# Optimization experiments

Measured on AMD Instinct MI355X. Metric: run time of the kernel, lower is better.

## Reference

```python
import jax, jax.numpy as jnp
import numpy as np


def _oct_table():
    # e_i * e_j = sgn[i,j] * e_{idx[i,j]}  (standard Fano-plane octonion table)
    idx = np.zeros((8, 8), dtype=np.int32)
    sgn = np.zeros((8, 8), dtype=np.float32)
    for j in range(8):
        idx[0, j] = j; sgn[0, j] = 1.0
    for i in range(1, 8):
        idx[i, 0] = i; sgn[i, 0] = 1.0
        idx[i, i] = 0; sgn[i, i] = -1.0
    for (a, b, c) in [(1, 2, 3), (1, 4, 5), (1, 7, 6), (2, 4, 6), (2, 5, 7), (3, 4, 7), (3, 6, 5)]:
        for (p, q, r) in ((a, b, c), (b, c, a), (c, a, b)):
            idx[p, q] = r; sgn[p, q] = 1.0
            idx[q, p] = r; sgn[q, p] = -1.0
    # For output part k and weight part i, J[k,i] is the unique input part j
    # with e_i*e_j = SG[k,i]*e_k.
    J = np.zeros((8, 8), dtype=np.int32)
    SG = np.zeros((8, 8), dtype=np.float32)
    for i in range(8):
        for j in range(8):
            k = idx[i, j]
            J[k, i] = j; SG[k, i] = sgn[i, j]
    return J, SG

_J, _SG = _oct_table()
_SGj = jnp.asarray(_SG)


def ternary_quant(W):
    # BitNet-style: per-matrix abs-mean scale, round+clip to {-1,0,1}, rescale.
    scale = jnp.mean(jnp.abs(W), axis=(1, 2), keepdims=True)
    return jnp.clip(jnp.round(W / (scale + 1e-8)), -1.0, 1.0) * scale


def oct_linear(x, W):
    # x: [B,T,Cin] (8 concatenated parts), W: [8, Pout, Pin]
    B, T, Cin = x.shape
    xp = x.reshape(B, T, 8, Cin // 8)
    Wq = ternary_quant(W)
    outs = []
    for k in range(8):  # fixed structural loop over octonion components
        xm = _SGj[k][None, None, :, None] * xp[:, :, _J[k], :]  # [B,T,8,Pin]
        outs.append(jnp.einsum('btip,iop->bto', xm, Wq))
    return jnp.concatenate(outs, axis=-1)  # [B,T,8*Pout]


def rmsnorm(x, w, eps=1e-6):
    return x * jax.lax.rsqrt(jnp.mean(x * x, axis=-1, keepdims=True) + eps) * w


def rope(x, cos, sin):
    # x: [B,T,H,D] with complex pairs (even, odd); cos/sin: [T,D/2]
    xr, xi = x[..., 0::2], x[..., 1::2]
    c = cos[None, :, None, :]
    s = sin[None, :, None, :]
    out_r = xr * c - xi * s
    out_i = xr * s + xi * c
    return jnp.stack([out_r, out_i], axis=-1).reshape(x.shape)


def setup_inputs() -> dict:
    B, T, C, H = 4, 1024, 2048, 16
    HD = C // H            # 128
    HIDDEN = 5464          # ceil(int(2*4*C/3)/8)*8
    key = jax.random.key(0)
    ks = jax.random.split(key, 10)
    x = jax.random.normal(ks[0], (B, T, C), jnp.float32)
    theta = 10000.0
    freqs = 1.0 / (theta ** (np.arange(0, HD, 2, dtype=np.float32) / HD))
    ang = np.arange(T, dtype=np.float32)[:, None] * freqs[None, :]
    w = lambda k, shape: jax.random.normal(k, shape, jnp.float32) * 0.02
    return {
        'x': x,
        'freqs_cos': jnp.asarray(np.cos(ang), jnp.float32),
        'freqs_sin': jnp.asarray(np.sin(ang), jnp.float32),
        'attn_norm_w': jnp.ones((C,), jnp.float32),
        'ffn_norm_w': jnp.ones((C,), jnp.float32),
        'wq': w(ks[1], (8, C // 8, C // 8)),
        'wk': w(ks[2], (8, C // 8, C // 8)),
        'wv': w(ks[3], (8, C // 8, C // 8)),
        'wo': w(ks[4], (8, C // 8, C // 8)),
        'w_gate': w(ks[5], (8, HIDDEN // 8, C // 8)),
        'w_up': w(ks[6], (8, HIDDEN // 8, C // 8)),
        'w_down': w(ks[7], (8, C // 8, HIDDEN // 8)),
    }


def reference(x, freqs_cos, freqs_sin, attn_norm_w, ffn_norm_w,
              wq, wk, wv, wo, w_gate, w_up, w_down):
    B, T, C = x.shape
    H = 16
    HD = C // H
    # attention sub-block
    xn = rmsnorm(x, attn_norm_w)
    q = oct_linear(xn, wq).reshape(B, T, H, HD)
    k = oct_linear(xn, wk).reshape(B, T, H, HD)
    v = oct_linear(xn, wv).reshape(B, T, H, HD)
    q = rope(q, freqs_cos, freqs_sin)
    k = rope(k, freqs_cos, freqs_sin)
    q, k, v = (t.transpose(0, 2, 1, 3) for t in (q, k, v))  # [B,H,T,D]
    scores = jnp.einsum('bhqd,bhkd->bhqk', q, k) / jnp.sqrt(jnp.float32(HD))
    causal = jnp.tril(jnp.ones((T, T), dtype=bool))
    scores = jnp.where(causal[None, None], scores, jnp.float32(-1e30))
    att = jax.nn.softmax(scores, axis=-1)
    y = jnp.einsum('bhqk,bhkd->bhqd', att, v).transpose(0, 2, 1, 3).reshape(B, T, C)
    h = x + oct_linear(y, wo)
    # SwiGLU MLP sub-block
    hn = rmsnorm(h, ffn_norm_w)
    gate = oct_linear(hn, w_gate)
    up = oct_linear(hn, w_up)
    ff = oct_linear(jax.nn.silu(gate) * up, w_down)
    return h + ff
```

## Files before the change

### kernel.cpp

```cpp
#include <hip/hip_runtime.h>
#include <stdint.h>

typedef __bf16 bf16;
typedef __bf16 bf16x8 __attribute__((ext_vector_type(8)));
typedef float f32x4 __attribute__((ext_vector_type(4)));

typedef const uint32_t __attribute__((address_space(1))) guint_t;
typedef uint32_t __attribute__((address_space(3))) luint_t;

__device__ __forceinline__ void gload_lds16(const void* g, void* l) {
  __builtin_amdgcn_global_load_lds((guint_t*)g, (luint_t*)l, 16, 0, 0);
}

struct OctTab { int J[64]; float SG[64]; };
struct Ptr7 { const float* p[7]; int opsz[7]; };

__global__ void scales_zero(float* __restrict__ scales) {
  if (threadIdx.x < 56) scales[threadIdx.x] = 0.f;
}

__global__ __launch_bounds__(256) void scales_partial(Ptr7 t, float* __restrict__ scales) {
  int bx = blockIdx.x;
  int part = bx & 7, sl = bx >> 3;
  int ti = sl >> 3, i = sl & 7;
  int n = t.opsz[ti];
  int n4 = n >> 2, seg = n4 >> 3;
  const float4* base = (const float4*)(t.p[ti] + (size_t)i * n) + part * seg;
  float s = 0.f;
  for (int j = threadIdx.x; j < seg; j += 256) {
    float4 v = base[j];
    s += fabsf(v.x) + fabsf(v.y) + fabsf(v.z) + fabsf(v.w);
  }
#pragma unroll
  for (int off = 32; off >= 1; off >>= 1) s += __shfl_xor(s, off);
  __shared__ float red[4];
  int lane = threadIdx.x & 63, wvi = threadIdx.x >> 6;
  if (lane == 0) red[wvi] = s;
  __syncthreads();
  if (threadIdx.x == 0) atomicAdd(&scales[sl], red[0] + red[1] + red[2] + red[3]);
}

__global__ __launch_bounds__(256) void build_dense_kernel(
    const float* __restrict__ W, const float* __restrict__ scales, float inv_n,
    bf16* __restrict__ Wt, int O, int P, int ld, int rowOff, int total, OctTab tab) {
  int idx = blockIdx.x * 256 + threadIdx.x;
  if (idx >= total) return;
  int p = idx % P;
  int rest = idx / P;
  int o = rest % O;
  rest /= O;
  int i = rest & 7;
  int k = rest >> 3;
  float s = scales[i] * inv_n;
  float w = W[((size_t)i * O + o) * P + p];
  float q = rintf(w / (s + 1e-8f));
  q = fminf(1.f, fmaxf(-1.f, q)) * s;
  int j = tab.J[k * 8 + i];
  float sg = tab.SG[k * 8 + i];
  Wt[(size_t)(rowOff + k * O + o) * ld + j * P + p] = (bf16)(sg * q);
}

__global__ __launch_bounds__(256) void zero_pad_kernel(bf16* __restrict__ Wd) {
  int idx = blockIdx.x * 256 + threadIdx.x;
  if (idx >= 81920) return;
  int row = idx / 40, c = idx % 40;
  Wd[(size_t)row * 5504 + 5464 + c] = (bf16)0.f;
}

__global__ __launch_bounds__(256) void rmsnorm_kernel(
    const float* __restrict__ x, const float* __restrict__ w, bf16* __restrict__ out) {
  int row = blockIdx.x;
  int tid = threadIdx.x;
  const float4* xp = (const float4*)(x + (size_t)row * 2048);
  float4 a = xp[tid * 2], b = xp[tid * 2 + 1];
  float ss = a.x*a.x + a.y*a.y + a.z*a.z + a.w*a.w
           + b.x*b.x + b.y*b.y + b.z*b.z + b.w*b.w;
#pragma unroll
  for (int off = 32; off >= 1; off >>= 1) ss += __shfl_xor(ss, off);
  __shared__ float red[4];
  int lane = tid & 63, wvi = tid >> 6;
  if (lane == 0) red[wvi] = ss;
  __syncthreads();
  float tot = red[0] + red[1] + red[2] + red[3];
  float rms = rsqrtf(tot * (1.f / 2048.f) + 1e-6f);
  const float4* wp = (const float4*)w;
  float4 wa = wp[tid * 2], wb = wp[tid * 2 + 1];
  bf16x8 ov;
  ov[0] = (bf16)(a.x * rms * wa.x); ov[1] = (bf16)(a.y * rms * wa.y);
  ov[2] = (bf16)(a.z * rms * wa.z); ov[3] = (bf16)(a.w * rms * wa.w);
  ov[4] = (bf16)(b.x * rms * wb.x); ov[5] = (bf16)(b.y * rms * wb.y);
  ov[6] = (bf16)(b.z * rms * wb.z); ov[7] = (bf16)(b.w * rms * wb.w);
  *(bf16x8*)(out + (size_t)row * 2048 + tid * 8) = ov;
}

template <int BM, int MODE, int SCHED>
__global__ __launch_bounds__(512, 2) void gemm_tile(
    const bf16* __restrict__ A, const bf16* __restrict__ Bt,
    const float* __restrict__ res, void* __restrict__ Cout,
    int K, int Nst, int ldC) {
  constexpr int ABYTES = BM * 128;
  constexpr int ACH = BM / 64;
  constexpr int TC  = ACH + 4;
  constexpr int MF  = BM / 32;
  constexpr int MFP = MF / 4;
  __shared__ char smem[2 * ABYTES + 65536];
  const int tid = threadIdx.x;
  const int lane = tid & 63, wave = tid >> 6;
  int nwg = gridDim.x * gridDim.y;
  int lin = blockIdx.y * gridDim.x + blockIdx.x;
  if ((nwg & 7) == 0) lin = (lin & 7) * (nwg >> 3) + (lin >> 3);
  const int bm = (lin / gridDim.x) * BM;
  const int bn = (lin % gridDim.x) * 256;
  const int wm = wave >> 2, wn = wave & 3;
  const int r = lane & 15, g = lane >> 4;
  const int srow = lane >> 3, sslot = lane & 7;

  f32x4 acc[MF][4] = {};
  const int nkt = K >> 6;

  auto STAGE = [&](int kt, int buf) {
    int k0 = kt << 6;
#pragma unroll
    for (int c = 0; c < ACH; ++c) {
      int ca = wave * ACH + c;
      int row = ca * 8 + srow;
      int sc = ((sslot ^ (row & 7)) << 3);
      gload_lds16(A + (size_t)(bm + row) * K + k0 + sc,
                  smem + buf * ABYTES + ca * 1024);
    }
#pragma unroll
    for (int c = 0; c < 4; ++c) {
      int cb = wave * 4 + c;
      int row = cb * 8 + srow;
      int sc = ((sslot ^ (row & 7)) << 3);
      gload_lds16(Bt + (size_t)(bn + row) * K + k0 + sc,
                  smem + 2 * ABYTES + buf * 32768 + cb * 1024);
    }
  };

  STAGE(0, 0);
  int cur = 0;
  for (int kt = 0; kt < nkt; ++kt) {
    if (kt + 1 < nkt) {
      STAGE(kt + 1, cur ^ 1);
      if constexpr (TC == 8) asm volatile("s_waitcnt vmcnt(8)" ::: "memory");
      else                   asm volatile("s_waitcnt vmcnt(6)" ::: "memory");
    } else {
      asm volatile("s_waitcnt vmcnt(0)" ::: "memory");
    }
    __builtin_amdgcn_s_barrier();
    const char* ab = smem + cur * ABYTES;
    const char* bb = smem + 2 * ABYTES + cur * 32768;
    bf16x8 bfr[4][2];
#pragma unroll
    for (int p = 0; p < 4; ++p) {
      if (p == 0) {
#pragma unroll
        for (int n = 0; n < 4; ++n)
#pragma unroll
          for (int kk = 0; kk < 2; ++kk) {
            int rown = wn * 64 + n * 16 + r;
            int cc = (kk * 4 + g) ^ (rown & 7);
            bfr[n][kk] = *(const bf16x8*)(bb + rown * 128 + cc * 16);
          }
      }
      bf16x8 af[MFP][2];
#pragma unroll
      for (int q = 0; q < MFP; ++q)
#pragma unroll
        for (int kk = 0; kk < 2; ++kk) {
          int rowm = wm * (BM / 2) + (p * MFP + q) * 16 + r;
          int cc = (kk * 4 + g) ^ (rowm & 7);
          af[q][kk] = *(const bf16x8*)(ab + rowm * 128 + cc * 16);
        }
      if constexpr (SCHED == 0) __builtin_amdgcn_s_barrier();
      __builtin_amdgcn_s_setprio(1);
#pragma unroll
      for (int q = 0; q < MFP; ++q)
#pragma unroll
        for (int n = 0; n < 4; ++n)
#pragma unroll
          for (int kk = 0; kk < 2; ++kk)
            acc[p * MFP + q][n] = __builtin_amdgcn_mfma_f32_16x16x32_bf16(
                af[q][kk], bfr[n][kk], acc[p * MFP + q][n], 0, 0, 0);
      __builtin_amdgcn_s_setprio(0);
      if constexpr (SCHED == 0) __builtin_amdgcn_s_barrier();
    }
    if constexpr (SCHED == 1) __builtin_amdgcn_s_barrier();
    cur ^= 1;
  }
#pragma unroll
  for (int mf = 0; mf < MF; ++mf) {
    int row0 = bm + wm * (BM / 2) + mf * 16 + g * 4;
#pragma unroll
    for (int nf = 0; nf < 4; ++nf) {
      int col = bn + wn * 64 + nf * 16 + r;
      if (col < Nst) {
#pragma unroll
        for (int j = 0; j < 4; ++j) {
          size_t off = (size_t)(row0 + j) * ldC + col;
          if (MODE == 0) ((bf16*)Cout)[off] = (bf16)acc[mf][nf][j];
          else           ((float*)Cout)[off] = acc[mf][nf][j] + res[off];
        }
      }
    }
  }
}

__global__ __launch_bounds__(256) void rope_kernel(
    bf16* __restrict__ qkv, const float* __restrict__ fc, const float* __restrict__ fs) {
  int tid = blockIdx.x * 256 + threadIdx.x;
  int ub = tid & 15;
  int h = (tid >> 4) & 15;
  int qk = (tid >> 8) & 1;
  int row = tid >> 9;
  int t = row & 1023;
  bf16* p = qkv + (size_t)row * 6144 + qk * 2048 + h * 128 + ub * 8;
  bf16x8 v = *(bf16x8*)p;
  const float4 cv = *(const float4*)(fc + t * 64 + ub * 4);
  const float4 sv = *(const float4*)(fs + t * 64 + ub * 4);
  float cr[4] = {cv.x, cv.y, cv.z, cv.w};
  float sr[4] = {sv.x, sv.y, sv.z, sv.w};
  bf16x8 ov;
#pragma unroll
  for (int u = 0; u < 4; ++u) {
    float xr = (float)v[2 * u], xi = (float)v[2 * u + 1];
    ov[2 * u]     = (bf16)(xr * cr[u] - xi * sr[u]);
    ov[2 * u + 1] = (bf16)(xr * sr[u] + xi * cr[u]);
  }
  *(bf16x8*)p = ov;
}

__global__ __launch_bounds__(256) void attn_kernel(
    const bf16* __restrict__ qkv, bf16* __restrict__ y) {
  __shared__ bf16 Vt[128][40];
  __shared__ bf16 P[4][16][40];
  int tid = threadIdx.x;
  int lane = tid & 63, wvi = tid >> 6;
  int bh = blockIdx.x, qt = blockIdx.y;
  int b = bh >> 4, h = bh & 15;
  int q0 = qt * 64;
  int r = lane & 15, g = lane >> 4;
  const bf16* base = qkv + (size_t)b * 1024 * 6144;
  bf16x8 qf[4];
  {
    const bf16* qp = base + (size_t)(q0 + wvi * 16 + r) * 6144 + h * 128 + g * 8;
#pragma unroll
    for (int kk = 0; kk < 4; ++kk) qf[kk] = *(const bf16x8*)(qp + kk * 32);
  }
  f32x4 o[8];
#pragma unroll
  for (int d = 0; d < 8; ++d) o[d] = (f32x4){0.f, 0.f, 0.f, 0.f};
  float m_run[4], l_run[4];
#pragma unroll
  for (int j = 0; j < 4; ++j) { m_run[j] = -1e30f; l_run[j] = 0.f; }
  const float sc = 0.08838834764831845f;
  int nch = (q0 >> 5) + 2;
  for (int c = 0; c < nch; ++c) {
    __syncthreads();
#pragma unroll
    for (int it = 0; it < 2; ++it) {
      int e = it * 256 + tid;
      int vr = e >> 4, dg = e & 15;
      bf16x8 vvv = *(const bf16x8*)(base + (size_t)(c * 32 + vr) * 6144 + 4096 + h * 128 + dg * 8);
      int ub = vr >> 3, uo = vr & 7;
#pragma unroll
      for (int u = 0; u < 8; ++u) {
        int R = dg * 8 + u;
        Vt[R][((ub ^ ((R >> 3) & 3)) << 3) + uo] = vvv[u];
      }
    }
    __syncthreads();
    f32x4 s0 = {0, 0, 0, 0}, s1 = {0, 0, 0, 0};
    const bf16* kp = base + (size_t)(c * 32 + r) * 6144 + 2048 + h * 128 + g * 8;
#pragma unroll
    for (int kk = 0; kk < 4; ++kk) {
      bf16x8 kf0 = *(const bf16x8*)(kp + kk * 32);
      bf16x8 kf1 = *(const bf16x8*)(kp + (size_t)16 * 6144 + kk * 32);
      s0 = __builtin_amdgcn_mfma_f32_16x16x32_bf16(qf[kk], kf0, s0, 0, 0, 0);
      s1 = __builtin_amdgcn_mfma_f32_16x16x32_bf16(qf[kk], kf1, s1, 0, 0, 0);
    }
    int qrow = q0 + wvi * 16 + g * 4;
    int kc = c * 32 + r;
    float pmax[4];
#pragma unroll
    for (int j = 0; j < 4; ++j) {
      float a0 = s0[j] * sc, a1 = s1[j] * sc;
      if (kc > qrow + j) a0 = -1e30f;
      if (kc + 16 > qrow + j) a1 = -1e30f;
      s0[j] = a0; s1[j] = a1;
      pmax[j] = fmaxf(a0, a1);
    }
#pragma unroll
    for (int j = 0; j < 4; ++j) {
#pragma unroll
      for (int w = 8; w >= 1; w >>= 1) pmax[j] = fmaxf(pmax[j], __shfl_xor(pmax[j], w));
    }
    float corr[4], rsum[4];
#pragma unroll
    for (int j = 0; j < 4; ++j) {
      float nm = fmaxf(m_run[j], pmax[j]);
      corr[j] = __expf(m_run[j] - nm);
      m_run[j] = nm;
      float p0 = __expf(s0[j] - nm), p1 = __expf(s1[j] - nm);
      s0[j] = p0; s1[j] = p1;
      rsum[j] = p0 + p1;
    }
#pragma unroll
    for (int j = 0; j < 4; ++j) {
#pragma unroll
      for (int w = 8; w >= 1; w >>= 1) rsum[j] += __shfl_xor(rsum[j], w);
      l_run[j] = l_run[j] * corr[j] + rsum[j];
      P[wvi][g * 4 + j][r] = (bf16)s0[j];
      P[wvi][g * 4 + j][16 + r] = (bf16)s1[j];
    }
#pragma unroll
    for (int d = 0; d < 8; ++d)
#pragma unroll
      for (int j = 0; j < 4; ++j) o[d][j] *= corr[j];
    asm volatile("s_waitcnt lgkmcnt(0)" ::: "memory");
    bf16x8 pa = *(const bf16x8*)&P[wvi][r][g * 8];
#pragma unroll
    for (int d = 0; d < 8; ++d) {
      int R = d * 16 + r;
      bf16x8 vb = *(const bf16x8*)&Vt[R][(g ^ ((R >> 3) & 3)) << 3];
      o[d] = __builtin_amdgcn_mfma_f32_16x16x32_bf16(pa, vb, o[d], 0, 0, 0);
    }
  }
#pragma unroll
  for (int j = 0; j < 4; ++j) {
    float inv = 1.f / l_run[j];
    size_t row = (size_t)(b * 1024 + q0 + wvi * 16 + g * 4 + j);
    bf16* yp = y + row * 2048 + h * 128 + r;
#pragma unroll
    for (int d = 0; d < 8; ++d) yp[d * 16] = (bf16)(o[d][j] * inv);
  }
}

__global__ __launch_bounds__(256) void silu_kernel(
    const bf16* __restrict__ up, bf16* __restrict__ gate_act) {
  int tid = blockIdx.x * 256 + threadIdx.x;
  int jb = tid % 688;
  int row = tid / 688;
  size_t off = (size_t)row * 5504 + jb * 8;
  bf16x8 ov;
  if (jb < 683) {
    bf16x8 gv = *(const bf16x8*)(gate_act + off);
    bf16x8 uv = *(const bf16x8*)(up + off);
#pragma unroll
    for (int u = 0; u < 8; ++u) {
      float gg = (float)gv[u], uu = (float)uv[u];
      ov[u] = (bf16)(gg / (1.f + __expf(-gg)) * uu);
    }
  } else {
#pragma unroll
    for (int u = 0; u < 8; ++u) ov[u] = (bf16)0.f;
  }
  *(bf16x8*)(gate_act + off) = ov;
}

static void build_oct(OctTab& t) {
  int idx[8][8]; float sgn[8][8];
  for (int j = 0; j < 8; ++j) { idx[0][j] = j; sgn[0][j] = 1.f; }
  for (int i = 1; i < 8; ++i) {
    idx[i][0] = i; sgn[i][0] = 1.f;
    idx[i][i] = 0; sgn[i][i] = -1.f;
  }
  const int tr[7][3] = {{1,2,3},{1,4,5},{1,7,6},{2,4,6},{2,5,7},{3,4,7},{3,6,5}};
  for (int ti = 0; ti < 7; ++ti) {
    int a = tr[ti][0], b = tr[ti][1], c = tr[ti][2];
    int cyc[3][3] = {{a,b,c},{b,c,a},{c,a,b}};
    for (int ci = 0; ci < 3; ++ci) {
      int p = cyc[ci][0], q = cyc[ci][1], r = cyc[ci][2];
      idx[p][q] = r; sgn[p][q] = 1.f;
      idx[q][p] = r; sgn[q][p] = -1.f;
    }
  }
  for (int i = 0; i < 8; ++i)
    for (int j = 0; j < 8; ++j) {
      int k = idx[i][j];
      t.J[k * 8 + i] = j;
      t.SG[k * 8 + i] = sgn[i][j];
    }
}

#define OFF_SCALES 0ull
#define OFF_WBUF   256ull
#define OFF_R16    (OFF_WBUF + 25165824ull)
#define OFF_QKVR   (OFF_R16 + 16777216ull)
#define OFF_H      (OFF_QKVR + 50331648ull)
#define OFF_G1     (OFF_H + 33554432ull)
#define WS_NEED    (OFF_G1 + 45088768ull)

extern "C" void kernel_launch(void* const* d_in, const int* in_sizes, int n_in,
                              void* d_out, int out_size, void* d_ws, size_t ws_size,
                              hipStream_t stream) {
  (void)in_sizes; (void)n_in; (void)out_size;
  if (ws_size < WS_NEED) return;

  const float* x   = (const float*)d_in[0];
  const float* fc  = (const float*)d_in[1];
  const float* fs  = (const float*)d_in[2];
  const float* anw = (const float*)d_in[3];
  const float* fnw = (const float*)d_in[4];
  const float* wqw = (const float*)d_in[5];
  const float* wkw = (const float*)d_in[6];
  const float* wvw = (const float*)d_in[7];
  const float* wow = (const float*)d_in[8];
  const float* wgw = (const float*)d_in[9];
  const float* wuw = (const float*)d_in[10];
  const float* wdw = (const float*)d_in[11];

  char* ws = (char*)d_ws;
  float* scales = (float*)(ws + OFF_SCALES);
  bf16* Wbuf = (bf16*)(ws + OFF_WBUF);
  bf16* xn   = (bf16*)(ws + OFF_R16);
  bf16* qkv  = (bf16*)(ws + OFF_QKVR);
  float* h   = (float*)(ws + OFF_H);
  bf16* g1   = (bf16*)(ws + OFF_G1);

  OctTab tab; build_oct(tab);
  Ptr7 p7;
  p7.p[0] = wqw; p7.p[1] = wkw; p7.p[2] = wvw; p7.p[3] = wow;
  p7.p[4] = wgw; p7.p[5] = wuw; p7.p[6] = wdw;
  for (int i = 0; i < 4; ++i) p7.opsz[i] = 65536;
  for (int i = 4; i < 7; ++i) p7.opsz[i] = 174848;

  const float invS = 1.f / 65536.f;
  const float invL = 1.f / 174848.f;

  scales_zero<<<1, 64, 0, stream>>>(scales);
  scales_partial<<<448, 256, 0, stream>>>(p7, scales);

  build_dense_kernel<<<16384, 256, 0, stream>>>(wqw, scales + 0,  invS, Wbuf, 256, 256, 2048, 0,    4194304, tab);
  build_dense_kernel<<<16384, 256, 0, stream>>>(wkw, scales + 8,  invS, Wbuf, 256, 256, 2048, 2048, 4194304, tab);
  build_dense_kernel<<<16384, 256, 0, stream>>>(wvw, scales + 16, invS, Wbuf, 256, 256, 2048, 4096, 4194304, tab);
  rmsnorm_kernel<<<4096, 256, 0, stream>>>(x, anw, xn);
  gemm_tile<128, 0, 0><<<dim3(24, 32), 512, 0, stream>>>(xn, Wbuf, nullptr, qkv, 2048, 6144, 6144);
  rope_kernel<<<8192, 256, 0, stream>>>(qkv, fc, fs);
  attn_kernel<<<dim3(64, 16), 256, 0, stream>>>(qkv, (bf16*)(ws + OFF_R16) );

  build_dense_kernel<<<16384, 256, 0, stream>>>(wow, scales + 24, invS, Wbuf, 256, 256, 2048, 0, 4194304, tab);
  gemm_tile<128, 1, 0><<<dim3(8, 32), 512, 0, stream>>>((bf16*)(ws + OFF_R16), Wbuf, x, h, 2048, 2048, 2048);

  bf16* hn = (bf16*)(ws + OFF_R16);
  rmsnorm_kernel<<<4096, 256, 0, stream>>>(h, fnw, hn);
  build_dense_kernel<<<43712, 256, 0, stream>>>(wgw, scales + 32, invL, Wbuf, 683, 256, 2048, 0, 11190272, tab);
  gemm_tile<128, 0, 1><<<dim3(22, 32), 512, 0, stream>>>(hn, Wbuf, nullptr, g1, 2048, 5504, 5504);
  bf16* up = (bf16*)(ws + OFF_QKVR);
  build_dense_kernel<<<43712, 256, 0, stream>>>(wuw, scales + 40, invL, Wbuf, 683, 256, 2048, 0, 11190272, tab);
  gemm_tile<128, 0, 0><<<dim3(22, 32), 512, 0, stream>>>(hn, Wbuf, nullptr, up, 2048, 5504, 5504);
  silu_kernel<<<11008, 256, 0, stream>>>(up, g1);
  build_dense_kernel<<<43712, 256, 0, stream>>>(wdw, scales + 48, invL, Wbuf, 256, 683, 5504, 0, 11190272, tab);
  zero_pad_kernel<<<320, 256, 0, stream>>>(Wbuf);
  gemm_tile<128, 1, 0><<<dim3(8, 32), 512, 0, stream>>>(g1, Wbuf, h, (float*)d_out, 5504, 2048, 2048);
}
```

Before: 921.8 us.

## Add triple-buffered LDS pipeline variant to GEMM for QKV and gate projections

```diff
diff --git a/kernel.cpp b/kernel.cpp
--- a/kernel.cpp
+++ b/kernel.cpp
@@ -103,7 +103,10 @@
   constexpr int TC  = ACH + 4;
   constexpr int MF  = BM / 32;
   constexpr int MFP = MF / 4;
-  __shared__ char smem[2 * ABYTES + 65536];
+  constexpr int NBUF = (SCHED == 2) ? 3 : 2;
+  __shared__ char smem[NBUF * (ABYTES + 32768)];
+  char* const Abase = smem;
+  char* const Bbase = smem + NBUF * ABYTES;
   const int tid = threadIdx.x;
   const int lane = tid & 63, wave = tid >> 6;
   int nwg = gridDim.x * gridDim.y;
@@ -126,7 +129,7 @@
       int row = ca * 8 + srow;
       int sc = ((sslot ^ (row & 7)) << 3);
       gload_lds16(A + (size_t)(bm + row) * K + k0 + sc,
-                  smem + buf * ABYTES + ca * 1024);
+                  Abase + buf * ABYTES + ca * 1024);
     }
 #pragma unroll
     for (int c = 0; c < 4; ++c) {
@@ -134,23 +137,11 @@
       int row = cb * 8 + srow;
       int sc = ((sslot ^ (row & 7)) << 3);
       gload_lds16(Bt + (size_t)(bn + row) * K + k0 + sc,
-                  smem + 2 * ABYTES + buf * 32768 + cb * 1024);
+                  Bbase + buf * 32768 + cb * 1024);
     }
   };
 
-  STAGE(0, 0);
-  int cur = 0;
-  for (int kt = 0; kt < nkt; ++kt) {
-    if (kt + 1 < nkt) {
-      STAGE(kt + 1, cur ^ 1);
-      if constexpr (TC == 8) asm volatile("s_waitcnt vmcnt(8)" ::: "memory");
-      else                   asm volatile("s_waitcnt vmcnt(6)" ::: "memory");
-    } else {
-      asm volatile("s_waitcnt vmcnt(0)" ::: "memory");
-    }
-    __builtin_amdgcn_s_barrier();
-    const char* ab = smem + cur * ABYTES;
-    const char* bb = smem + 2 * ABYTES + cur * 32768;
+  auto COMPUTE = [&](const char* ab, const char* bb) {
     bf16x8 bfr[4][2];
 #pragma unroll
     for (int p = 0; p < 4; ++p) {
@@ -186,9 +177,47 @@
       __builtin_amdgcn_s_setprio(0);
       if constexpr (SCHED == 0) __builtin_amdgcn_s_barrier();
     }
-    if constexpr (SCHED == 1) __builtin_amdgcn_s_barrier();
-    cur ^= 1;
-  }
+  };
+
+  if constexpr (SCHED == 2) {
+    STAGE(0, 0);
+    if (nkt > 1) STAGE(1, 1);
+    int b = 0;
+    for (int kt = 0; kt < nkt; ++kt) {
+      if (kt + 2 < nkt) STAGE(kt + 2, (b + 2 >= 3) ? b - 1 : b + 2);
+      int rem = nkt - 1 - kt;
+      if (rem >= 2) {
+        if constexpr (TC == 6) asm volatile("s_waitcnt vmcnt(12)" ::: "memory");
+        else                   asm volatile("s_waitcnt vmcnt(16)" ::: "memory");
+      } else if (rem == 1) {
+        if constexpr (TC == 6) asm volatile("s_waitcnt vmcnt(6)" ::: "memory");
+        else                   asm volatile("s_waitcnt vmcnt(8)" ::: "memory");
+      } else {
+        asm volatile("s_waitcnt vmcnt(0)" ::: "memory");
+      }
+      __builtin_amdgcn_s_barrier();
+      COMPUTE(Abase + b * ABYTES, Bbase + b * 32768);
+      __builtin_amdgcn_s_barrier();
+      b = (b + 1 == 3) ? 0 : b + 1;
+    }
+  } else {
+    STAGE(0, 0);
+    int cur = 0;
+    for (int kt = 0; kt < nkt; ++kt) {
+      if (kt + 1 < nkt) {
+        STAGE(kt + 1, cur ^ 1);
+        if constexpr (TC == 8) asm volatile("s_waitcnt vmcnt(8)" ::: "memory");
+        else                   asm volatile("s_waitcnt vmcnt(6)" ::: "memory");
+      } else {
+        asm volatile("s_waitcnt vmcnt(0)" ::: "memory");
+      }
+      __builtin_amdgcn_s_barrier();
+      COMPUTE(Abase + cur * ABYTES, Bbase + cur * 32768);
+      if constexpr (SCHED == 1) __builtin_amdgcn_s_barrier();
+      cur ^= 1;
+    }
+  }
+
 #pragma unroll
   for (int mf = 0; mf < MF; ++mf) {
     int row0 = bm + wm * (BM / 2) + mf * 16 + g * 4;
@@ -436,7 +465,7 @@
   build_dense_kernel<<<16384, 256, 0, stream>>>(wkw, scales + 8,  invS, Wbuf, 256, 256, 2048, 2048, 4194304, tab);
   build_dense_kernel<<<16384, 256, 0, stream>>>(wvw, scales + 16, invS, Wbuf, 256, 256, 2048, 4096, 4194304, tab);
   rmsnorm_kernel<<<4096, 256, 0, stream>>>(x, anw, xn);
-  gemm_tile<128, 0, 0><<<dim3(24, 32), 512, 0, stream>>>(xn, Wbuf, nullptr, qkv, 2048, 6144, 6144);
+  gemm_tile<128, 0, 2><<<dim3(24, 32), 512, 0, stream>>>(xn, Wbuf, nullptr, qkv, 2048, 6144, 6144);
   rope_kernel<<<8192, 256, 0, stream>>>(qkv, fc, fs);
   attn_kernel<<<dim3(64, 16), 256, 0, stream>>>(qkv, (bf16*)(ws + OFF_R16) );
 
@@ -446,7 +475,7 @@
   bf16* hn = (bf16*)(ws + OFF_R16);
   rmsnorm_kernel<<<4096, 256, 0, stream>>>(h, fnw, hn);
   build_dense_kernel<<<43712, 256, 0, stream>>>(wgw, scales + 32, invL, Wbuf, 683, 256, 2048, 0, 11190272, tab);
-  gemm_tile<128, 0, 1><<<dim3(22, 32), 512, 0, stream>>>(hn, Wbuf, nullptr, g1, 2048, 5504, 5504);
+  gemm_tile<128, 0, 2><<<dim3(22, 32), 512, 0, stream>>>(hn, Wbuf, nullptr, g1, 2048, 5504, 5504);
   bf16* up = (bf16*)(ws + OFF_QKVR);
   build_dense_kernel<<<43712, 256, 0, stream>>>(wuw, scales + 40, invL, Wbuf, 683, 256, 2048, 0, 11190272, tab);
   gemm_tile<128, 0, 0><<<dim3(22, 32), 512, 0, stream>>>(hn, Wbuf, nullptr, up, 2048, 5504, 5504);
```

Measured after the change: 913.1 us. Within noise of the previous version (-0.9%).
